# Kernel tuning notes

Hardware: AMD Instinct MI355X
Metric: run time of the kernel (lower is better)

Reference implementation:

```python
import jax, jax.numpy as jnp
import numpy as np

DIM = 512
CODEBOOK_SIZE = 8192
B, N = 4, 4096


def setup_inputs() -> dict:
    key = jax.random.key(0)
    k1, k2, k3 = jax.random.split(key, 3)
    scale = DIM ** -0.5
    x = jax.random.normal(k1, (B, N, DIM), dtype=jnp.float32)
    codebook = jax.random.normal(k2, (CODEBOOK_SIZE, DIM), dtype=jnp.float32) * scale
    W = jax.random.normal(k3, (DIM, DIM), dtype=jnp.float32) * scale  # Linear(dim, dim, bias=False) weight
    return {"x": x, "codebook": codebook, "W": W}


def reference(x, codebook, W):
    # implicit_codebook = Linear(codebook): codebook @ W.T   -> [C, D]
    implicit = codebook @ W.T

    # nearest-code search (no grad in original): squared euclidean distance
    x_sg = jax.lax.stop_gradient(x)
    imp_sg = jax.lax.stop_gradient(implicit)
    # [B, N, C] logits; ||x||^2 constant w.r.t. argmin so omitted
    d2 = jnp.sum(imp_sg * imp_sg, axis=-1) - 2.0 * jnp.einsum("bnd,cd->bnc", x_sg, imp_sg)
    indices = jnp.argmin(d2, axis=-1)  # [B, N]

    quantized = implicit[indices]  # gather [B, N, D]

    commit_loss = (
        0.25 * jnp.mean((x - jax.lax.stop_gradient(quantized)) ** 2)
        + jnp.mean((jax.lax.stop_gradient(x) - quantized) ** 2)
    )

    # straight-through estimator
    quantized_st = jax.lax.stop_gradient(quantized - x) + x
    return quantized_st, indices, commit_loss
```

## Files before the change

### kernel.cpp

```cpp
#include <hip/hip_runtime.h>
#include <stdint.h>

#define DIM 512
#define NCODE 8192
#define NTOK 16384
#define QELEMS (NTOK * DIM)
#define IDX_OFF QELEMS
#define LOSS_OFF (QELEMS + NTOK)

#define S_X 21.166666f
#define S_I 423.33334f
#define SXSI 8960.5551f
#define NQ_BIAS 131072
#define MARGIN_INT 3136

#define OFF_NORMS ((size_t)NCODE * DIM * 4)
#define OFF_XI8   (OFF_NORMS + (size_t)NCODE * 4)
#define OFF_II8   (OFF_XI8 + (size_t)NTOK * DIM)
#define OFF_CAND  (OFF_II8 + (size_t)NCODE * DIM)
#define OFF_NQ    (OFF_CAND + (size_t)NTOK * 64 * 4 * 4)

typedef short bf16x8 __attribute__((ext_vector_type(8)));
typedef float f32x4 __attribute__((ext_vector_type(4)));
typedef int   i32x4 __attribute__((ext_vector_type(4)));

__device__ inline unsigned ord32(float f) {
    unsigned u = __float_as_uint(f);
    return (u & 0x80000000u) ? ~u : (u | 0x80000000u);
}
__device__ inline unsigned short f2bf(float f) {
    unsigned u = __float_as_uint(f);
    return (unsigned short)((u + 0x7fffu + ((u >> 16) & 1u)) >> 16);
}
__device__ inline float bf2f(unsigned short h) {
    return __uint_as_float((unsigned)h << 16);
}
__device__ inline int q8(float v, float s) {
    return __float2int_rn(fminf(fmaxf(v * s, -127.f), 127.f));
}
__device__ inline void gl_lds16(const void* g, void* l) {
    __builtin_amdgcn_global_load_lds(
        (const __attribute__((address_space(1))) void*)g,
        (__attribute__((address_space(3))) void*)l, 16, 0, 0);
}

__device__ inline void leaf4(const uint4 v, unsigned r[4]) {
    const unsigned s0 = min(v.x, v.z), t0 = max(v.x, v.z);
    const unsigned s1 = min(v.y, v.w), t1 = max(v.y, v.w);
    r[0] = s0; r[1] = min(t0, s1); r[2] = max(t0, s1); r[3] = t1;
}
__device__ inline void merge44(unsigned a[4], const unsigned b[4]) {
    const unsigned h0 = min(a[0], b[3]), h1 = min(a[1], b[2]);
    const unsigned h2 = min(a[2], b[1]), h3 = min(a[3], b[0]);
    const unsigned l0 = min(h0, h2), u0 = max(h0, h2);
    const unsigned l1 = min(h1, h3), u1 = max(h1, h3);
    a[0] = min(l0, l1); a[1] = max(l0, l1);
    a[2] = min(u0, u1); a[3] = max(u0, u1);
}

__global__ void init_kernel(float* __restrict__ norms) {
    int i = blockIdx.x * blockDim.x + threadIdx.x;
    if (i < NCODE) norms[i] = 0.f;
}

__global__ void split_kernel(const float* __restrict__ src,
                             unsigned short* __restrict__ dst, int n4) {
    int i = blockIdx.x * blockDim.x + threadIdx.x;
    if (i >= n4) return;
    float4 v = ((const float4*)src)[i];
    int r = i >> 7;
    int c = (i & 127) << 2;
    unsigned short hx = f2bf(v.x), hy = f2bf(v.y), hz = f2bf(v.z), hw = f2bf(v.w);
    ushort4 hi = {hx, hy, hz, hw};
    ushort4 lo = {f2bf(v.x - bf2f(hx)), f2bf(v.y - bf2f(hy)),
                  f2bf(v.z - bf2f(hz)), f2bf(v.w - bf2f(hw))};
    *(ushort4*)(dst + (size_t)r * 1024 + c) = hi;
    *(ushort4*)(dst + (size_t)r * 1024 + 512 + c) = lo;
}

__global__ __launch_bounds__(256, 2)
void gemm_imp_kernel(const unsigned short* __restrict__ A2,
                     const unsigned short* __restrict__ B2,
                     float* __restrict__ imp, unsigned char* __restrict__ impi8,
                     float* __restrict__ norms) {
    __shared__ __align__(16) unsigned short As2[64 * 64];
    __shared__ __align__(16) unsigned short Bs2[128 * 64];
    const int tid = threadIdx.x;
    const int l = tid & 63;
    const int w = tid >> 6;
    const int row0 = blockIdx.y * 64;
    const int col0 = blockIdx.x * 128;
    const int lr = l & 15;
    const int q = l >> 4;

    const int rr8 = l >> 3;
    const int gch = (l & 7) ^ (rr8 & 7);

    const unsigned short* gA = A2 + (size_t)(row0 + w * 8 + rr8) * 1024 + gch * 8;
    const unsigned short* gB = B2 + (size_t)(col0 + w * 8 + rr8) * 1024 + gch * 8;
    unsigned short* lA = As2 + (w * 8) * 64;
    unsigned short* lB = Bs2 + (w * 8) * 64;

    f32x4 acc[4][2];
    #pragma unroll
    for (int i = 0; i < 4; ++i)
        #pragma unroll
        for (int j = 0; j < 2; ++j) acc[i][j] = (f32x4)0.f;

    for (int c = 0; c < 32; ++c) {
        const int kA = (c & 15) << 6;
        const int kB = (c < 16) ? kA : ((kA + 512) & 1023);
        #pragma unroll
        for (int s = 0; s < 2; ++s)
            gl_lds16(gA + (size_t)(s * 32) * 1024 + kA, lA + (s * 32) * 64);
        #pragma unroll
        for (int s = 0; s < 4; ++s)
            gl_lds16(gB + (size_t)(s * 32) * 1024 + kB, lB + (s * 32) * 64);
        __syncthreads();
        #pragma unroll
        for (int ks = 0; ks < 2; ++ks) {
            const int lc = ks * 4 + q;
            bf16x8 af[4], bf[2];
            #pragma unroll
            for (int i = 0; i < 4; ++i) {
                const int ra = i * 16 + lr;
                af[i] = *(const bf16x8*)(As2 + ra * 64 + ((lc ^ (ra & 7)) << 3));
            }
            #pragma unroll
            for (int j = 0; j < 2; ++j) {
                const int rb = w * 32 + j * 16 + lr;
                bf[j] = *(const bf16x8*)(Bs2 + rb * 64 + ((lc ^ (rb & 7)) << 3));
            }
            #pragma unroll
            for (int i = 0; i < 4; ++i)
                #pragma unroll
                for (int j = 0; j < 2; ++j)
                    acc[i][j] = __builtin_amdgcn_mfma_f32_16x16x32_bf16(
                        af[i], bf[j], acc[i][j], 0, 0, 0);
        }
        __syncthreads();
    }

    #pragma unroll
    for (int i = 0; i < 4; ++i) {
        float np[4] = {0.f, 0.f, 0.f, 0.f};
        #pragma unroll
        for (int j = 0; j < 2; ++j) {
            const int col = col0 + w * 32 + j * 16 + lr;
            #pragma unroll
            for (int r = 0; r < 4; ++r) {
                const int row = row0 + i * 16 + q * 4 + r;
                const float v = acc[i][j][r];
                imp[(size_t)row * DIM + col] = v;
                impi8[(size_t)row * DIM + col] = (unsigned char)(q8(v, S_I) & 0xff);
                np[r] = fmaf(v, v, np[r]);
            }
        }
        #pragma unroll
        for (int r = 0; r < 4; ++r) {
            float s = np[r];
            #pragma unroll
            for (int m = 1; m < 16; m <<= 1) s += __shfl_xor(s, m, 64);
            if (lr == 0)
                atomicAdd(&norms[row0 + i * 16 + q * 4 + r], s);
        }
    }
}

__global__ void cvtx_kernel(const float* __restrict__ src,
                            unsigned char* __restrict__ dst,
                            const float* __restrict__ norms,
                            int* __restrict__ norms_q, int n4) {
    int i = blockIdx.x * blockDim.x + threadIdx.x;
    if (i >= n4) return;
    if (i < NCODE) norms_q[i] = __float2int_rn(norms[i] * SXSI) + NQ_BIAS;
    float4 v = ((const float4*)src)[i];
    unsigned wd = (unsigned)(q8(v.x, S_X) & 0xff)
                | ((unsigned)(q8(v.y, S_X) & 0xff) << 8)
                | ((unsigned)(q8(v.z, S_X) & 0xff) << 16)
                | ((unsigned)(q8(v.w, S_X) & 0xff) << 24);
    ((unsigned*)dst)[i] = wd;
}

__global__ __launch_bounds__(256, 4)
void coarse_kernel(const unsigned char* __restrict__ Xi8,
                   const unsigned char* __restrict__ Ii8,
                   const int* __restrict__ norms_q,
                   unsigned* __restrict__ cand) {
    __shared__ __align__(16) unsigned char smem[32768];
    unsigned* Sw = (unsigned*)smem;

    const int tid = threadIdx.x;
    const int l = tid & 63;
    const int w = tid >> 6;

    const int id = blockIdx.y * 64 + blockIdx.x;
    const int xcd = id & 7;
    const int s8 = id >> 3;
    const int bx = xcd * 8 + (s8 & 7);
    const int by = s8 >> 3;
    const int row0 = by * 128;
    const int col0 = bx * 128;

    const int wm = w & 1, wn = w >> 1;
    const int lr = l & 15;
    const int q = l >> 4;

    const int sl = l >> 3;
    const int eq = (l & 7) ^ sl;
    const int se = eq >> 2;
    const int sq = eq & 3;
    const unsigned char* gA0 =
        Xi8 + (size_t)(row0 + 2 * (w * 8 + sl) + se) * DIM + sq * 16;
    const unsigned char* gB0 =
        Ii8 + (size_t)(col0 + 2 * (w * 8 + sl) + se) * DIM + sq * 16;
    const int ldsA = w * 1024;
    const int ldsB = 8192 + w * 1024;

    const int p8 = ((((lr & 1) << 2) | q) ^ ((lr >> 1) & 7)) << 4;
    const int rdA = (wm * 32 + (lr >> 1)) * 128 + p8;
    const int rdB = 8192 + (wn * 32 + (lr >> 1)) * 128 + p8;

    i32x4 acc[4][4];
    #pragma unroll
    for (int i = 0; i < 4; ++i)
        #pragma unroll
        for (int j = 0; j < 4; ++j) acc[i][j] = (i32x4)0;

    #pragma unroll
    for (int s = 0; s < 2; ++s) {
        gl_lds16(gA0 + (size_t)(s * 64) * DIM, smem + ldsA + s * 4096);
        gl_lds16(gB0 + (size_t)(s * 64) * DIM, smem + ldsB + s * 4096);
    }
    __syncthreads();

    #pragma unroll
    for (int it = 0; it < 8; ++it) {
        const int cb = (it & 1) * 16384;
        if (it < 7) {
            const int nb = ((it + 1) & 1) * 16384;
            const int kc = (it + 1) << 6;
            #pragma unroll
            for (int s = 0; s < 2; ++s) {
                gl_lds16(gA0 + (size_t)(s * 64) * DIM + kc, smem + nb + ldsA + s * 4096);
                gl_lds16(gB0 + (size_t)(s * 64) * DIM + kc, smem + nb + ldsB + s * 4096);
            }
        }
        i32x4 af[4], bfr[4];
        #pragma unroll
        for (int i = 0; i < 4; ++i)
            af[i] = *(const i32x4*)(smem + cb + rdA + i * 1024);
        #pragma unroll
        for (int j = 0; j < 4; ++j)
            bfr[j] = *(const i32x4*)(smem + cb + rdB + j * 1024);
        #pragma unroll
        for (int i = 0; i < 4; ++i)
            #pragma unroll
            for (int j = 0; j < 4; ++j)
                acc[i][j] = __builtin_amdgcn_mfma_i32_16x16x64_i8(
                    af[i], bfr[j], acc[i][j], 0, 0, 0);
        __syncthreads();
    }

    int nqo[4];
    unsigned codes[4];
    #pragma unroll
    for (int j = 0; j < 4; ++j) {
        codes[j] = (unsigned)(col0 + wn * 64 + j * 16 + lr);
        nqo[j] = norms_q[codes[j]];
    }
    const int c4w = wn * 8 + (lr >> 1);
    const int wsub = (lr & 1) << 1;
    #pragma unroll
    for (int i = 0; i < 4; ++i) {
        #pragma unroll
        for (int r = 0; r < 4; ++r) {
            unsigned pv[4];
            #pragma unroll
            for (int j = 0; j < 4; ++j) {
                int d2o = nqo[j] - 2 * acc[i][j][r];
                d2o = min(max(d2o, 0), 262143);
                pv[j] = ((unsigned)d2o << 13) | codes[j];
            }
            const unsigned s1 = min(pv[0], pv[1]), g1 = max(pv[0], pv[1]);
            const unsigned s2 = min(pv[2], pv[3]), g2 = max(pv[2], pv[3]);
            uint2 o;
            o.x = min(s1, s2);
            o.y = min(max(s1, s2), min(g1, g2));
            const int tok = wm * 64 + i * 16 + q * 4 + r;
            *(uint2*)(Sw + tok * 64 + ((c4w ^ (tok & 7)) << 2) + wsub) = o;
        }
    }
    __syncthreads();

    {
        const int t = tid >> 1, h = tid & 1;
        const unsigned* rowp = Sw + t * 64;
        const int sxor = t & 7;
        unsigned a4[4], b4[4];
        {
            const uint4 va = *(const uint4*)(rowp + (((h * 8 + 0) ^ sxor) << 2));
            const uint4 vb = *(const uint4*)(rowp + (((h * 8 + 1) ^ sxor) << 2));
            leaf4(va, a4); leaf4(vb, b4); merge44(a4, b4);
        }
        #pragma unroll
        for (int p = 1; p < 4; ++p) {
            unsigned c4a[4], c4b[4];
            const uint4 va = *(const uint4*)(rowp + (((h * 8 + 2 * p) ^ sxor) << 2));
            const uint4 vb = *(const uint4*)(rowp + (((h * 8 + 2 * p + 1) ^ sxor) << 2));
            leaf4(va, c4a); leaf4(vb, c4b); merge44(c4a, c4b);
            merge44(a4, c4a);
        }
        const unsigned p3 = (unsigned)__shfl_xor((int)a4[3], 1, 64);
        const unsigned p2 = (unsigned)__shfl_xor((int)a4[2], 1, 64);
        const unsigned u0 = min(a4[0], p3);
        const unsigned u1 = min(a4[1], p2);
        uint2 o2;
        o2.x = h ? u1 : u0;
        o2.y = h ? u0 : u1;
        *(uint2*)(cand + ((size_t)bx * NTOK + row0 + t) * 4 + h * 2) = o2;
    }
}

__global__ __launch_bounds__(256)
void merge_kernel(const float* __restrict__ X, const float* __restrict__ Imp,
                  const float* __restrict__ norms, const unsigned* __restrict__ cand,
                  float* __restrict__ out, float* __restrict__ lossp) {
    const int t = blockIdx.x * 4 + (threadIdx.x >> 6);
    const int l = threadIdx.x & 63;

    const uint4 c4 = *(const uint4*)(cand + ((size_t)l * NTOK + t) * 4);
    unsigned mn = min(min(c4.x, c4.y), min(c4.z, c4.w));
    #pragma unroll
    for (int o = 32; o > 0; o >>= 1)
        mn = min(mn, (unsigned)__shfl_xor((int)mn, o, 64));
    const unsigned th = (mn >> 13) + MARGIN_INT;

    const float4* xp = (const float4*)(X + (size_t)t * DIM);
    const float4 xa = xp[l * 2], xb = xp[l * 2 + 1];

    const unsigned vv[4] = {c4.x, c4.y, c4.z, c4.w};
    unsigned long long best = ~0ull;
    #pragma unroll
    for (int i = 0; i < 4; ++i) {
        const bool pass = (vv[i] >> 13) <= th;
        unsigned long long m = __ballot(pass);
        while (m) {
            const int src = __ffsll((unsigned long long)m) - 1;
            m &= m - 1;
            const int c = __shfl((int)(vv[i] & 8191u), src, 64);
            const float4* ip = (const float4*)(Imp + (size_t)c * DIM);
            const float4 ia = ip[l * 2], ib = ip[l * 2 + 1];
            float s = xa.x * ia.x + xa.y * ia.y + xa.z * ia.z + xa.w * ia.w
                    + xb.x * ib.x + xb.y * ib.y + xb.z * ib.z + xb.w * ib.w;
            #pragma unroll
            for (int o = 32; o > 0; o >>= 1) s += __shfl_xor(s, o, 64);
            const float d = fmaf(-2.f, s, norms[c]);
            const unsigned long long p =
                ((unsigned long long)ord32(d) << 32) | (unsigned)c;
            if (p < best) best = p;
        }
    }
    const int bi = (int)(best & 0xffffffffu);

    const float4* qp = (const float4*)(Imp + (size_t)bi * DIM);
    float4* op = (float4*)(out + (size_t)t * DIM);
    float ls = 0.f;
    #pragma unroll
    for (int jj = 0; jj < 2; ++jj) {
        const int j = l + jj * 64;
        const float4 qv = qp[j], xv = xp[j];
        op[j] = qv;
        const float dx = xv.x - qv.x, dy = xv.y - qv.y,
                    dz = xv.z - qv.z, dw = xv.w - qv.w;
        ls += dx * dx + dy * dy + dz * dz + dw * dw;
    }
    #pragma unroll
    for (int o = 32; o > 0; o >>= 1) ls += __shfl_xor(ls, o, 64);
    if (l == 0) {
        lossp[t] = ls;
        out[IDX_OFF + t] = (float)bi;
    }
}

__global__ __launch_bounds__(1024)
void fin_kernel(const float* __restrict__ lossp, float* __restrict__ out) {
    __shared__ float part[16];
    float s = 0.f;
    for (int i = threadIdx.x; i < NTOK; i += 1024) s += lossp[i];
    #pragma unroll
    for (int o = 32; o > 0; o >>= 1) s += __shfl_xor(s, o, 64);
    if ((threadIdx.x & 63) == 0) part[threadIdx.x >> 6] = s;
    __syncthreads();
    if (threadIdx.x == 0) {
        float tot = 0.f;
        #pragma unroll
        for (int i = 0; i < 16; ++i) tot += part[i];
        out[LOSS_OFF] = 1.25f * tot / (float)QELEMS;
    }
}

extern "C" void kernel_launch(void* const* d_in, const int* in_sizes, int n_in,
                              void* d_out, int out_size, void* d_ws, size_t ws_size,
                              hipStream_t stream) {
    const float* x  = (const float*)d_in[0];
    const float* cb = (const float*)d_in[1];
    const float* W  = (const float*)d_in[2];
    float* out = (float*)d_out;
    char* ws = (char*)d_ws;

    float* imp = (float*)ws;
    float* norms = (float*)(ws + OFF_NORMS);
    unsigned char* xi8 = (unsigned char*)(ws + OFF_XI8);
    unsigned char* ii8 = (unsigned char*)(ws + OFF_II8);
    unsigned* cand = (unsigned*)(ws + OFF_CAND);
    int* norms_q = (int*)(ws + OFF_NQ);
    unsigned short* cb2 = (unsigned short*)(ws + OFF_CAND);
    unsigned short* W2  = (unsigned short*)(ws + OFF_XI8);
    float* lossp = (float*)(ws + OFF_XI8);

    hipLaunchKernelGGL(init_kernel, dim3(NCODE / 256), dim3(256), 0, stream, norms);
    hipLaunchKernelGGL(split_kernel, dim3(NCODE * 128 / 256), dim3(256), 0, stream,
                       cb, cb2, NCODE * 128);
    hipLaunchKernelGGL(split_kernel, dim3(512 * 128 / 256), dim3(256), 0, stream,
                       W, W2, 512 * 128);
    hipLaunchKernelGGL(gemm_imp_kernel, dim3(DIM / 128, NCODE / 64), dim3(256), 0,
                       stream, cb2, W2, imp, ii8, norms);
    hipLaunchKernelGGL(cvtx_kernel, dim3(NTOK * DIM / 4 / 256), dim3(256), 0, stream,
                       x, xi8, norms, norms_q, NTOK * DIM / 4);
    hipLaunchKernelGGL(coarse_kernel, dim3(NCODE / 128, NTOK / 128), dim3(256), 0,
                       stream, xi8, ii8, norms_q, cand);
    hipLaunchKernelGGL(merge_kernel, dim3(NTOK / 4), dim3(256), 0, stream,
                       x, imp, norms, cand, out, lossp);
    hipLaunchKernelGGL(fin_kernel, dim3(1), dim3(1024), 0, stream, lossp, out);
}
```

Baseline: 273.9 us.

## Prefetch two stages ahead with explicit vmcnt waits in int8 distance GEMM

Restructures the double-buffered K loop of the int8 MFMA distance kernel so two stages of global-to-LDS loads are in flight at once. Each iteration waits with a partial vmcnt count instead of a full __syncthreads, uses raw s_barrier plus sched_barrier to pin instruction order, and refills the buffer it just consumed after a second barrier. The goal is to hide more global load latency behind the MFMAs. In exchange it depends on exact vmcnt accounting for the direct-to-LDS loads and adds a second barrier per iteration.

```diff
diff --git a/kernel.cpp b/kernel.cpp
--- a/kernel.cpp
+++ b/kernel.cpp
@@ -227,25 +227,26 @@
         #pragma unroll
         for (int j = 0; j < 4; ++j) acc[i][j] = (i32x4)0;
 
-    #pragma unroll
-    for (int s = 0; s < 2; ++s) {
-        gl_lds16(gA0 + (size_t)(s * 64) * DIM, smem + ldsA + s * 4096);
-        gl_lds16(gB0 + (size_t)(s * 64) * DIM, smem + ldsB + s * 4096);
-    }
-    __syncthreads();
+#define STAGE(buf, kc) do {                                                  \
+        gl_lds16(gA0 + (size_t)(kc),             smem + (buf) + ldsA);       \
+        gl_lds16(gA0 + (size_t)64 * DIM + (kc),  smem + (buf) + ldsA + 4096);\
+        gl_lds16(gB0 + (size_t)(kc),             smem + (buf) + ldsB);       \
+        gl_lds16(gB0 + (size_t)64 * DIM + (kc),  smem + (buf) + ldsB + 4096);\
+    } while (0)
+
+    STAGE(0, 0);
+    STAGE(16384, 64);
 
     #pragma unroll
     for (int it = 0; it < 8; ++it) {
         const int cb = (it & 1) * 16384;
         if (it < 7) {
-            const int nb = ((it + 1) & 1) * 16384;
-            const int kc = (it + 1) << 6;
-            #pragma unroll
-            for (int s = 0; s < 2; ++s) {
-                gl_lds16(gA0 + (size_t)(s * 64) * DIM + kc, smem + nb + ldsA + s * 4096);
-                gl_lds16(gB0 + (size_t)(s * 64) * DIM + kc, smem + nb + ldsB + s * 4096);
-            }
-        }
+            asm volatile("s_waitcnt vmcnt(4)" ::: "memory");
+        } else {
+            asm volatile("s_waitcnt vmcnt(0)" ::: "memory");
+        }
+        __builtin_amdgcn_s_barrier();
+        __builtin_amdgcn_sched_barrier(0);
         i32x4 af[4], bfr[4];
         #pragma unroll
         for (int i = 0; i < 4; ++i)
@@ -259,8 +260,14 @@
             for (int j = 0; j < 4; ++j)
                 acc[i][j] = __builtin_amdgcn_mfma_i32_16x16x64_i8(
                     af[i], bfr[j], acc[i][j], 0, 0, 0);
-        __syncthreads();
-    }
+        asm volatile("s_waitcnt lgkmcnt(0)" ::: "memory");
+        __builtin_amdgcn_sched_barrier(0);
+        __builtin_amdgcn_s_barrier();
+        if (it < 6) {
+            STAGE(cb, (it + 2) << 6);
+        }
+    }
+#undef STAGE
 
     int nqo[4];
     unsigned codes[4];
```

New measurement: 249.8 us. -8.8%, faster.
